# Kernel tuning notes

Hardware: AMD Instinct MI355X
Metric: run time of the kernel (lower is better)

## Reference

```python
import jax, jax.numpy as jnp
import numpy as np

B, S, W, MODES, NUM, NLAYERS = 32, 8192, 128, 16, 8, 4
LG = 8192 + 40 - 1  # szie + len - 1 (Gabor filter length)
PI = float(np.pi)


def setup_inputs() -> dict:
    key = jax.random.key(0)
    ks = jax.random.split(key, 10)
    scale = 1.0 / (W * W)
    return {
        "x": jax.random.normal(ks[0], (B, S, 1), jnp.float32),
        "w1_re": scale * jax.random.uniform(ks[1], (NLAYERS, W, W, MODES), jnp.float32),
        "w1_im": scale * jax.random.uniform(ks[2], (NLAYERS, W, W, MODES), jnp.float32),
        "gamma": jnp.tile(jnp.linspace(0.01, 0.02, NUM, dtype=jnp.float32)[None], (NLAYERS, 1)),
        "fwhm": jnp.tile(jnp.linspace(0.001, 0.002, NUM, dtype=jnp.float32)[None], (NLAYERS, 1)),
        "w2": jax.random.uniform(ks[3], (NLAYERS, NUM), jnp.float32),
        "cw": jax.random.normal(ks[4], (NLAYERS, W, W), jnp.float32) / np.sqrt(W),
        "cb": jnp.zeros((NLAYERS, W), jnp.float32),
        "fc0_w": jax.random.normal(ks[5], (W, 2), jnp.float32) / np.sqrt(2.0),
        "fc0_b": jnp.zeros((W,), jnp.float32),
        "fc1_w": jax.random.normal(ks[6], (128, W), jnp.float32) / np.sqrt(W),
        "fc1_b": jnp.zeros((128,), jnp.float32),
        "fc2_w": jax.random.normal(ks[7], (1, 128), jnp.float32) / np.sqrt(128.0),
        "fc2_b": jnp.zeros((1,), jnp.float32),
    }


def _spectral_conv(h, w_re, w_im, gamma, fwhm, w2):
    # h: [B, C, S] real. w_re/w_im: [C, C, MODES]. gamma/fwhm/w2: [NUM].
    u = jnp.linspace(-0.5, 0.5, LG, dtype=h.dtype)                      # [LG]
    t1 = (gamma * PI / (fwhm + 1e-5))[:, None]                          # [NUM,1]
    gab = jnp.exp(-(t1 ** 2) * (u[None, :] - fwhm[:, None]) ** 2)       # [NUM,LG]
    gab = jnp.fft.ifftshift(gab, axes=-1)[:, :MODES]                     # [NUM,MODES]
    # weights2 is a scalar per latent kernel -> fold the num-reduction into an
    # effective per-mode Gabor weight (exact same math as the repeated einsum + sum).
    g_eff = jnp.einsum("k,km->m", w2, gab)                               # [MODES]
    w1 = (w_re + 1j * w_im) * g_eff[None, None, :]                       # [C,C,MODES] complex
    xf = jnp.fft.rfft(h)                                                 # [B,C,F], F=S//2+1
    out_m = jnp.einsum("bim,iom->bom", xf[..., :MODES], w1)              # [B,C,MODES]
    out = jnp.zeros(xf.shape, dtype=xf.dtype).at[..., :MODES].set(out_m)
    return jnp.fft.irfft(out, n=h.shape[-1])                             # [B,C,S]


def reference(x, w1_re, w1_im, gamma, fwhm, w2, cw, cb, fc0_w, fc0_b, fc1_w, fc1_b, fc2_w, fc2_b):
    b, s, _ = x.shape
    grid = jnp.broadcast_to(jnp.linspace(0.0, 1.0, s, dtype=x.dtype)[None, :, None], (b, s, 1))
    h = jnp.concatenate([x, grid], axis=-1)                              # [B,S,2]
    h = h @ fc0_w.T + fc0_b                                              # [B,S,W]
    h = jnp.transpose(h, (0, 2, 1))                                      # [B,W,S]
    for l in range(NLAYERS):
        x1 = _spectral_conv(h, w1_re[l], w1_im[l], gamma[l], fwhm[l], w2[l])
        x2 = jnp.einsum("oi,bis->bos", cw[l], h) + cb[l][None, :, None]  # 1x1 conv
        h = x1 + x2
        if l < NLAYERS - 1:
            h = jax.nn.gelu(h, approximate=False)
    h = jnp.transpose(h, (0, 2, 1))                                      # [B,S,W]
    h = jax.nn.gelu(h @ fc1_w.T + fc1_b, approximate=False)              # [B,S,128]
    return h @ fc2_w.T + fc2_b                                           # [B,S,1]
```

## Files before the change

kernel.cpp:

```cpp
#include <hip/hip_runtime.h>
#include <hip/hip_fp16.h>

#define BB 32
#define SS 8192
#define CC 128
#define MM 16
#define NUMK 8
#define NL 4

#define TWO_PI 6.2831853071795864769f

typedef _Float16 f16x8 __attribute__((ext_vector_type(8)));
typedef float f32x4 __attribute__((ext_vector_type(4)));

#define MFMA16(a, b, c) __builtin_amdgcn_mfma_f32_16x16x32_f16((a), (b), (c), 0, 0, 0)

__device__ __forceinline__ float gelu_f(float v) {
    float u = 0.7978845608f * fmaf(0.044715f * v * v, v, v);
    float a = fabsf(u);
    float e = __expf(-2.0f * a);
    float th = __fdividef(1.0f - e, 1.0f + e);
    th = copysignf(th, u);
    return 0.5f * v * (1.0f + th);
}

__device__ __align__(256) __half g_trigA[SS * 32];
__device__ __align__(256) __half g_trigD[32 * SS];
__device__ __align__(256) __half g_cwh[NL * CC * CC];
__device__ __align__(256) __half g_fc1h[CC * CC];
__device__ __align__(256) __half g_omh[BB * CC * 32];
__device__ __align__(256) float  g_Xfp[BB * 64 * 32 * CC];
__device__ __align__(256) float  g_Xf[BB * 32 * CC];
__device__ __align__(256) float  g_Xx[BB * MM * 2];
__device__ __align__(256) float  g_Xg[MM * 2];

__global__ __launch_bounds__(256) void k_prep(const float* __restrict__ cw,
                                              const float* __restrict__ fc1_w) {
    int idx = blockIdx.x * 256 + threadIdx.x;
    if (idx < NL * CC * CC) g_cwh[idx] = __float2half(cw[idx]);
    if (idx < CC * CC)      g_fc1h[idx] = __float2half(fc1_w[idx]);
}

__global__ __launch_bounds__(256) void k_trig() {
    int s = blockIdx.x * 256 + threadIdx.x;
    for (int m = 0; m < MM; m++) {
        int ms = (m * s) & (SS - 1);
        float th = (float)ms * (TWO_PI / (float)SS);
        float sn, cs;
        sincosf(th, &sn, &cs);
        g_trigA[s * 32 + m]        = __float2half(cs);
        g_trigA[s * 32 + 16 + m]   = __float2half(sn);
        g_trigD[m * SS + s]        = __float2half(cs);
        g_trigD[(16 + m) * SS + s] = __float2half(-sn);
    }
}

__global__ __launch_bounds__(256) void k_dftx(const float* __restrict__ x) {
    __shared__ float red[4][MM][2];
    int blk = blockIdx.x;
    int t = threadIdx.x;
    int lane = t & 63;
    int wv = t >> 6;

    float accR[MM], accI[MM], cr[MM], ci[MM], pc[MM], ps[MM];
#pragma unroll
    for (int m = 0; m < MM; m++) {
        float sn, cs;
        sincosf((TWO_PI / (float)SS) * (float)(m * t), &sn, &cs);
        cr[m] = cs; ci[m] = -sn;
        sincosf((TWO_PI * 256.0f / (float)SS) * (float)m, &sn, &cs);
        pc[m] = cs; ps[m] = -sn;
        accR[m] = 0.f; accI[m] = 0.f;
    }
    for (int k = 0; k < 32; k++) {
        int s = t + (k << 8);
        float v = (blk < BB) ? x[(blk << 13) + s] : (float)s * (1.0f / 8191.0f);
#pragma unroll
        for (int m = 0; m < MM; m++) {
            accR[m] = fmaf(v, cr[m], accR[m]);
            accI[m] = fmaf(v, ci[m], accI[m]);
            float nc = cr[m] * pc[m] - ci[m] * ps[m];
            float ns = cr[m] * ps[m] + ci[m] * pc[m];
            cr[m] = nc; ci[m] = ns;
        }
    }
#pragma unroll
    for (int m = 0; m < MM; m++) {
#pragma unroll
        for (int off = 32; off > 0; off >>= 1) {
            accR[m] += __shfl_xor(accR[m], off, 64);
            accI[m] += __shfl_xor(accI[m], off, 64);
        }
        if (lane == 0) { red[wv][m][0] = accR[m]; red[wv][m][1] = accI[m]; }
    }
    __syncthreads();
    if (t < MM * 2) {
        int m = t >> 1, p = t & 1;
        float s = red[0][m][p] + red[1][m][p] + red[2][m][p] + red[3][m][p];
        if (blk < BB) g_Xx[(blk << 5) + (m << 1) + p] = s;
        else          g_Xg[(m << 1) + p] = s;
    }
}

__global__ __launch_bounds__(256) void k_xf0(const float* __restrict__ fc0_w,
                                             const float* __restrict__ fc0_b) {
    int n = blockIdx.x * 256 + threadIdx.x;
    int i = n & 127, m2 = (n >> 7) & 31, b = n >> 12;
    int m = m2 & 15, p = m2 >> 4;
    float xv = g_Xx[(b << 5) + (m << 1) + p];
    float gv = g_Xg[(m << 1) + p];
    float v = fc0_w[2 * i] * xv + fc0_w[2 * i + 1] * gv;
    if (p == 0 && m == 0) v += (float)SS * fc0_b[i];
    g_Xf[(b << 12) + (m2 << 7) + i] = v;
}

__global__ __launch_bounds__(256) void k_fc0(const float* __restrict__ x,
                                             const float* __restrict__ fc0_w,
                                             const float* __restrict__ fc0_b,
                                             __half* __restrict__ h) {
    int idx = blockIdx.x * 256 + threadIdx.x;
    int wq = idx & 15;
    int s = (idx >> 4) & (SS - 1);
    int b = idx >> 17;
    float g = (float)s * (1.0f / (float)(SS - 1));
    float xv = x[(b << 13) + s];
    union { __half2 q[4]; f16x8 v; } pk;
#pragma unroll
    for (int j = 0; j < 4; j++) {
        int w = wq * 8 + j * 2;
        float4 fw = *(const float4*)(fc0_w + 2 * w);
        float2 fb = *(const float2*)(fc0_b + w);
        float v0 = fmaf(fw.x, xv, fmaf(fw.y, g, fb.x));
        float v1 = fmaf(fw.z, xv, fmaf(fw.w, g, fb.y));
        pk.q[j] = __floats2half2_rn(v0, v1);
    }
    *(f16x8*)((char*)h + ((long)idx << 4)) = pk.v;
}

__global__ __launch_bounds__(256) void k_red2() {
    int n = blockIdx.x * 256 + threadIdx.x;
    int i = n & 127, m2 = (n >> 7) & 31, b = n >> 12;
    const float* p = g_Xfp + (((b << 6) << 5) + (m2 << 7)) + i;
    float s = 0.f;
#pragma unroll 8
    for (int t = 0; t < 64; t++) s += p[t << 12];
    g_Xf[(b << 12) + (m2 << 7) + i] = s;
}

__global__ __launch_bounds__(256) void k_mix(const float* __restrict__ w1_re,
                                             const float* __restrict__ w1_im,
                                             const float* __restrict__ gamma,
                                             const float* __restrict__ fwhm,
                                             const float* __restrict__ w2,
                                             const float* __restrict__ cb, int l) {
    __shared__ float geff[MM];
    int t = threadIdx.x;
    if (t < MM) {
        float g = 0.f;
        for (int k = 0; k < NUMK; k++) {
            float fw = fwhm[l * NUMK + k];
            float t1 = gamma[l * NUMK + k] * 3.14159265358979f / (fw + 1e-5f);
            float u = (float)t * (1.0f / 8230.0f) - fw;
            g = fmaf(w2[l * NUMK + k], expf(-t1 * t1 * u * u), g);
        }
        geff[t] = g;
    }
    __syncthreads();

    int n = blockIdx.x * 256 + t;
    int m = n & 15, o = (n >> 4) & 127, b = n >> 11;
    const float* xr = g_Xf + (b << 12) + (m << 7);
    const float* xi = g_Xf + (b << 12) + ((16 + m) << 7);
    const float* wr = w1_re + (l << 18) + (o << 4) + m;
    const float* wi = w1_im + (l << 18) + (o << 4) + m;
    float orr = 0.f, oii = 0.f;
    for (int i = 0; i < CC; i++) {
        float xrv = xr[i], xiv = xi[i];
        float wrv = wr[i << 11], wiv = wi[i << 11];
        orr = fmaf(xrv, wrv, orr); orr = fmaf(-xiv, wiv, orr);
        oii = fmaf(xrv, wiv, oii); oii = fmaf(xiv, wrv, oii);
    }
    float sc = geff[m] * (2.0f / (float)SS) * ((m == 0) ? 0.5f : 1.0f);
    float base = (m == 0) ? cb[l * CC + o] : 0.0f;
    g_omh[(b << 12) + (o << 5) + m]      = __float2half(orr * sc + base);
    g_omh[(b << 12) + (o << 5) + 16 + m] = __float2half(-oii * sc);
}

#define GEMM_STEP(KS, HA, HB)                                                       \
    _Pragma("unroll")                                                               \
    for (int af = 0; af < 8; af++) {                                                \
        int row = (af << 4) + lr;                                                   \
        const f16x8 av = *(const f16x8*)(ldsA + (row << 8) +                        \
                          ((((KS << 2) + lg) ^ (row & 7)) << 4));                   \
        acc[af][0] = MFMA16(av, HA, acc[af][0]);                                    \
        acc[af][1] = MFMA16(av, HB, acc[af][1]);                                    \
    }

#define LOAD_HF(S0X)                                                                \
    {                                                                               \
        int hr = (((b << 13) + (S0X) + (wid << 5) + lr) << 8) + (lg << 4);          \
        hf0 = *(const f16x8*)(h_c + hr);                                            \
        hf1 = *(const f16x8*)(h_c + hr + (16 << 8));                                \
        hf2 = *(const f16x8*)(h_c + hr + (1 << 6));                                 \
        hf3 = *(const f16x8*)(h_c + hr + (16 << 8) + (1 << 6));                     \
        hf4 = *(const f16x8*)(h_c + hr + (2 << 6));                                 \
        hf5 = *(const f16x8*)(h_c + hr + (16 << 8) + (2 << 6));                     \
        hf6 = *(const f16x8*)(h_c + hr + (3 << 6));                                 \
        hf7 = *(const f16x8*)(h_c + hr + (16 << 8) + (3 << 6));                     \
    }

#define LOAD_TF(S0X)                                                                \
    {                                                                               \
        int tr2 = (((S0X) + (wid << 5) + lr) << 6) + (lg << 4);                     \
        tf0 = *(const f16x8*)(ta_c + tr2);                                          \
        tf1 = *(const f16x8*)(ta_c + tr2 + (16 << 6));                              \
    }

template <int TAIL>
__global__ __launch_bounds__(256, 2) void k_layer(__half* __restrict__ h, int l) {
    __shared__ __align__(16) char smem[TAIL ? 73728 : 40960];
    char* ldsA = smem;
    char* ldsO = smem + 32768;
    char* ldsS = smem + (TAIL ? 40960 : 0);
    int bi = blockIdx.x;
    int b = bi >> 4, grp = bi & 15;
    int Sg = grp << 9;
    int t = threadIdx.x;
    int wid = __builtin_amdgcn_readfirstlane(t >> 6);
    int l6 = t & 63, lr = l6 & 15, lg = l6 >> 4;
    const char* h_c = (const char*)h;
    char* hw = (char*)h;
    const char* cw_c = (const char*)(g_cwh + l * CC * CC);
    const char* om_c = (const char*)(g_omh + (b << 12));
    const char* ta_c = (const char*)g_trigA;
    const char* td_c = (const char*)g_trigD;
    char* strip = ldsS + (wid << 13);

#pragma unroll
    for (int k = 0; k < 8; k++) {
        int c = (k << 8) + t;
        f16x8 v = *(const f16x8*)(cw_c + (c << 4));
        int row = c >> 4, c16 = c & 15;
        *(f16x8*)(ldsA + (row << 8) + ((c16 ^ (row & 7)) << 4)) = v;
    }
#pragma unroll
    for (int k = 0; k < 2; k++) {
        int c = (k << 8) + t;
        f16x8 v = *(const f16x8*)(om_c + (c << 4));
        int row = c >> 2, c4 = c & 3;
        *(f16x8*)(ldsO + (row << 6) + ((c4 ^ (row & 3)) << 4)) = v;
    }
    f16x8 hf0, hf1, hf2, hf3, hf4, hf5, hf6, hf7, tf0, tf1;
    LOAD_HF(Sg)
    LOAD_TF(Sg)
    __syncthreads();

    f32x4 dacc[8][2];
    if (TAIL) {
#pragma unroll
        for (int af = 0; af < 8; af++) {
            dacc[af][0] = (f32x4){0.f, 0.f, 0.f, 0.f};
            dacc[af][1] = (f32x4){0.f, 0.f, 0.f, 0.f};
        }
    }

    for (int ti = 0; ti < 4; ti++) {
        int S0 = Sg + (ti << 7);
        f32x4 acc[8][2];
#pragma unroll
        for (int af = 0; af < 8; af++) {
            acc[af][0] = (f32x4){0.f, 0.f, 0.f, 0.f};
            acc[af][1] = (f32x4){0.f, 0.f, 0.f, 0.f};
        }
        __builtin_amdgcn_s_setprio(1);
        GEMM_STEP(0, hf0, hf1)
        GEMM_STEP(1, hf2, hf3)
        GEMM_STEP(2, hf4, hf5)
        GEMM_STEP(3, hf6, hf7)
#pragma unroll
        for (int af = 0; af < 8; af++) {
            int row = (af << 4) + lr;
            const f16x8 ov = *(const f16x8*)(ldsO + (row << 6) + ((lg ^ (row & 3)) << 4));
            acc[af][0] = MFMA16(ov, tf0, acc[af][0]);
            acc[af][1] = MFMA16(ov, tf1, acc[af][1]);
        }
        __builtin_amdgcn_s_setprio(0);
        if (ti < 3) {
            int S0n = S0 + 128;
            LOAD_HF(S0n)
            LOAD_TF(S0n)
        }
        f16x8 td0, td1;
        if (TAIL) {
            int sgl = S0 + (wid << 5) + (lg << 3);
            td0 = *(const f16x8*)(td_c + (((lr << 13) + sgl) << 1));
            td1 = *(const f16x8*)(td_c + ((((16 + lr) << 13) + sgl) << 1));
        }
#pragma unroll
        for (int bf = 0; bf < 2; bf++) {
            int s_w = (bf << 4) + lr;
            int s = S0 + (wid << 5) + s_w;
#pragma unroll
            for (int af = 0; af < 8; af++) {
                int o0 = (af << 4) + (lg << 2);
                float v0 = acc[af][bf][0], v1 = acc[af][bf][1];
                float v2 = acc[af][bf][2], v3 = acc[af][bf][3];
                if (TAIL) { v0 = gelu_f(v0); v1 = gelu_f(v1); v2 = gelu_f(v2); v3 = gelu_f(v3); }
                union { __half2 q[2]; unsigned long long u; } pk;
                pk.q[0] = __floats2half2_rn(v0, v1);
                pk.q[1] = __floats2half2_rn(v2, v3);
                *(unsigned long long*)(hw + (((b << 13) + s) << 8) + (o0 << 1)) = pk.u;
                if (TAIL) {
                    int byte = (s_w << 8) + ((o0 << 1) ^ ((s_w & 15) << 4));
                    *(unsigned long long*)(strip + byte) = pk.u;
                }
            }
        }
        if (TAIL) {
            asm volatile("s_waitcnt lgkmcnt(0)" ::: "memory");
            __builtin_amdgcn_sched_barrier(0);
#pragma unroll
            for (int af = 0; af < 8; af++) {
                int o = (af << 4) + lr;
                union { unsigned int u[4]; f16x8 v; } bb;
#pragma unroll
                for (int p = 0; p < 4; p++) {
                    int s0 = (lg << 3) + 2 * p, s1 = s0 + 1;
                    unsigned int lo = *(const unsigned short*)
                        (strip + (s0 << 8) + ((o << 1) ^ ((s0 & 15) << 4)));
                    unsigned int hi = *(const unsigned short*)
                        (strip + (s1 << 8) + ((o << 1) ^ ((s1 & 15) << 4)));
                    bb.u[p] = lo | (hi << 16);
                }
                dacc[af][0] = MFMA16(td0, bb.v, dacc[af][0]);
                dacc[af][1] = MFMA16(td1, bb.v, dacc[af][1]);
            }
        }
    }
    if (TAIL) {
        float* xp = g_Xfp + (((b << 6) + (grp << 2) + wid) << 12);
#pragma unroll
        for (int af = 0; af < 8; af++)
#pragma unroll
            for (int mh = 0; mh < 2; mh++)
#pragma unroll
                for (int reg = 0; reg < 4; reg++) {
                    int m2 = (mh << 4) + (lg << 2) + reg;
                    int o = (af << 4) + lr;
                    xp[(m2 << 7) + o] = dacc[af][mh][reg];
                }
    }
}

__global__ __launch_bounds__(256) void k_head(const __half* __restrict__ h,
                                              const float* __restrict__ fc1_b,
                                              const float* __restrict__ fc2_w,
                                              const float* __restrict__ fc2_b,
                                              float* __restrict__ out) {
    __shared__ __align__(16) char smem[32768];
    char* ldsA = smem;
    int bi = blockIdx.x;
    int b = bi >> 4, grp = bi & 15;
    int Sg = grp << 9;
    int t = threadIdx.x;
    int wid = __builtin_amdgcn_readfirstlane(t >> 6);
    int l6 = t & 63, lr = l6 & 15, lg = l6 >> 4;
    const char* h_c = (const char*)h;
    const char* f1_c = (const char*)g_fc1h;

#pragma unroll
    for (int k = 0; k < 8; k++) {
        int c = (k << 8) + t;
        f16x8 v = *(const f16x8*)(f1_c + (c << 4));
        int row = c >> 4, c16 = c & 15;
        *(f16x8*)(ldsA + (row << 8) + ((c16 ^ (row & 7)) << 4)) = v;
    }
    f16x8 hf0, hf1, hf2, hf3, hf4, hf5, hf6, hf7;
    LOAD_HF(Sg)
    __syncthreads();

    float f2b = fc2_b[0];
    for (int ti = 0; ti < 4; ti++) {
        int S0 = Sg + (ti << 7);
        f32x4 acc[8][2];
#pragma unroll
        for (int af = 0; af < 8; af++) {
            acc[af][0] = (f32x4){0.f, 0.f, 0.f, 0.f};
            acc[af][1] = (f32x4){0.f, 0.f, 0.f, 0.f};
        }
        __builtin_amdgcn_s_setprio(1);
        GEMM_STEP(0, hf0, hf1)
        GEMM_STEP(1, hf2, hf3)
        GEMM_STEP(2, hf4, hf5)
        GEMM_STEP(3, hf6, hf7)
        __builtin_amdgcn_s_setprio(0);
        if (ti < 3) { LOAD_HF(S0 + 128) }
        float p[2] = {0.f, 0.f};
#pragma unroll
        for (int af = 0; af < 8; af++) {
            float4 fb = *(const float4*)(fc1_b + (af << 4) + (lg << 2));
            float4 f2 = *(const float4*)(fc2_w + (af << 4) + (lg << 2));
#pragma unroll
            for (int bf = 0; bf < 2; bf++) {
                float v0 = gelu_f(acc[af][bf][0] + fb.x);
                float v1 = gelu_f(acc[af][bf][1] + fb.y);
                float v2 = gelu_f(acc[af][bf][2] + fb.z);
                float v3 = gelu_f(acc[af][bf][3] + fb.w);
                p[bf] += f2.x * v0 + f2.y * v1 + f2.z * v2 + f2.w * v3;
            }
        }
#pragma unroll
        for (int bf = 0; bf < 2; bf++) {
            float v = p[bf];
            v += __shfl_xor(v, 16, 64);
            v += __shfl_xor(v, 32, 64);
            if (lg == 0) out[(b << 13) + S0 + (wid << 5) + (bf << 4) + lr] = v + f2b;
        }
    }
}

extern "C" void kernel_launch(void* const* d_in, const int* in_sizes, int n_in,
                              void* d_out, int out_size, void* d_ws, size_t ws_size,
                              hipStream_t stream) {
    const float* x      = (const float*)d_in[0];
    const float* w1_re  = (const float*)d_in[1];
    const float* w1_im  = (const float*)d_in[2];
    const float* gamma  = (const float*)d_in[3];
    const float* fwhm   = (const float*)d_in[4];
    const float* w2     = (const float*)d_in[5];
    const float* cw     = (const float*)d_in[6];
    const float* cb     = (const float*)d_in[7];
    const float* fc0_w  = (const float*)d_in[8];
    const float* fc0_b  = (const float*)d_in[9];
    const float* fc1_w  = (const float*)d_in[10];
    const float* fc1_b  = (const float*)d_in[11];
    const float* fc2_w  = (const float*)d_in[12];
    const float* fc2_b  = (const float*)d_in[13];
    float* out = (float*)d_out;

    __half* h = (__half*)d_ws;

    k_prep<<<dim3(256), dim3(256), 0, stream>>>(cw, fc1_w);
    k_trig<<<dim3(32), dim3(256), 0, stream>>>();
    k_dftx<<<dim3(33), dim3(256), 0, stream>>>(x);
    k_xf0<<<dim3(512), dim3(256), 0, stream>>>(fc0_w, fc0_b);
    k_fc0<<<dim3(16384), dim3(256), 0, stream>>>(x, fc0_w, fc0_b, h);
    for (int l = 0; l < NL; l++) {
        k_mix<<<dim3(256), dim3(256), 0, stream>>>(w1_re, w1_im, gamma, fwhm, w2, cb, l);
        if (l < NL - 1) {
            k_layer<1><<<dim3(512), dim3(256), 0, stream>>>(h, l);
            k_red2<<<dim3(512), dim3(256), 0, stream>>>();
        } else {
            k_layer<0><<<dim3(512), dim3(256), 0, stream>>>(h, l);
        }
    }
    k_head<<<dim3(512), dim3(256), 0, stream>>>(h, fc1_b, fc2_w, fc2_b, out);
}
```

Measured before the change: 342.3 us.

## Fuse last layer with head and stage h stores through LDS for coalescing

The final spectral layer and the fc1/gelu/fc2 head are merged into one kernel. The layer output stays in an LDS strip as fp16 and feeds the fc1 MFMA directly, so the last full write and re-read of h in global memory goes away, along with one launch. In the non-final layers, h is now written back from the swizzled LDS strip as 16-byte rows instead of scattered 8-byte stores. The cost is that fc1 weights are read from global/L2 inside the inner loop, and the extra LDS readback adds latency.

```diff
diff --git a/kernel.cpp b/kernel.cpp
--- a/kernel.cpp
+++ b/kernel.cpp
@@ -216,12 +216,11 @@
         tf1 = *(const f16x8*)(ta_c + tr2 + (16 << 6));                              \
     }
 
-template <int TAIL>
 __global__ __launch_bounds__(256, 2) void k_layer(__half* __restrict__ h, int l) {
-    __shared__ __align__(16) char smem[TAIL ? 73728 : 40960];
+    __shared__ __align__(16) char smem[73728];
     char* ldsA = smem;
     char* ldsO = smem + 32768;
-    char* ldsS = smem + (TAIL ? 40960 : 0);
+    char* ldsS = smem + 40960;
     int bi = blockIdx.x;
     int b = bi >> 4, grp = bi & 15;
     int Sg = grp << 9;
@@ -256,12 +255,10 @@
     __syncthreads();
 
     f32x4 dacc[8][2];
-    if (TAIL) {
-#pragma unroll
-        for (int af = 0; af < 8; af++) {
-            dacc[af][0] = (f32x4){0.f, 0.f, 0.f, 0.f};
-            dacc[af][1] = (f32x4){0.f, 0.f, 0.f, 0.f};
-        }
+#pragma unroll
+    for (int af = 0; af < 8; af++) {
+        dacc[af][0] = (f32x4){0.f, 0.f, 0.f, 0.f};
+        dacc[af][1] = (f32x4){0.f, 0.f, 0.f, 0.f};
     }
 
     for (int ti = 0; ti < 4; ti++) {
@@ -291,7 +288,7 @@
             LOAD_TF(S0n)
         }
         f16x8 td0, td1;
-        if (TAIL) {
+        {
             int sgl = S0 + (wid << 5) + (lg << 3);
             td0 = *(const f16x8*)(td_c + (((lr << 13) + sgl) << 1));
             td1 = *(const f16x8*)(td_c + ((((16 + lr) << 13) + sgl) << 1));
@@ -299,45 +296,44 @@
 #pragma unroll
         for (int bf = 0; bf < 2; bf++) {
             int s_w = (bf << 4) + lr;
-            int s = S0 + (wid << 5) + s_w;
 #pragma unroll
             for (int af = 0; af < 8; af++) {
                 int o0 = (af << 4) + (lg << 2);
-                float v0 = acc[af][bf][0], v1 = acc[af][bf][1];
-                float v2 = acc[af][bf][2], v3 = acc[af][bf][3];
-                if (TAIL) { v0 = gelu_f(v0); v1 = gelu_f(v1); v2 = gelu_f(v2); v3 = gelu_f(v3); }
+                float v0 = gelu_f(acc[af][bf][0]), v1 = gelu_f(acc[af][bf][1]);
+                float v2 = gelu_f(acc[af][bf][2]), v3 = gelu_f(acc[af][bf][3]);
                 union { __half2 q[2]; unsigned long long u; } pk;
                 pk.q[0] = __floats2half2_rn(v0, v1);
                 pk.q[1] = __floats2half2_rn(v2, v3);
-                *(unsigned long long*)(hw + (((b << 13) + s) << 8) + (o0 << 1)) = pk.u;
-                if (TAIL) {
-                    int byte = (s_w << 8) + ((o0 << 1) ^ ((s_w & 15) << 4));
-                    *(unsigned long long*)(strip + byte) = pk.u;
-                }
-            }
-        }
-        if (TAIL) {
-            asm volatile("s_waitcnt lgkmcnt(0)" ::: "memory");
-            __builtin_amdgcn_sched_barrier(0);
-#pragma unroll
-            for (int af = 0; af < 8; af++) {
-                int o = (af << 4) + lr;
-                union { unsigned int u[4]; f16x8 v; } bb;
-#pragma unroll
-                for (int p = 0; p < 4; p++) {
-                    int s0 = (lg << 3) + 2 * p, s1 = s0 + 1;
-                    unsigned int lo = *(const unsigned short*)
-                        (strip + (s0 << 8) + ((o << 1) ^ ((s0 & 15) << 4)));
-                    unsigned int hi = *(const unsigned short*)
-                        (strip + (s1 << 8) + ((o << 1) ^ ((s1 & 15) << 4)));
-                    bb.u[p] = lo | (hi << 16);
-                }
-                dacc[af][0] = MFMA16(td0, bb.v, dacc[af][0]);
-                dacc[af][1] = MFMA16(td1, bb.v, dacc[af][1]);
-            }
-        }
-    }
-    if (TAIL) {
+                int byte = (s_w << 8) + ((o0 << 1) ^ ((s_w & 15) << 4));
+                *(unsigned long long*)(strip + byte) = pk.u;
+            }
+        }
+        asm volatile("s_waitcnt lgkmcnt(0)" ::: "memory");
+        __builtin_amdgcn_sched_barrier(0);
+#pragma unroll
+        for (int af = 0; af < 8; af++) {
+            int o = (af << 4) + lr;
+            union { unsigned int u[4]; f16x8 v; } bb;
+#pragma unroll
+            for (int p = 0; p < 4; p++) {
+                int s0 = (lg << 3) + 2 * p, s1 = s0 + 1;
+                unsigned int lo = *(const unsigned short*)
+                    (strip + (s0 << 8) + ((o << 1) ^ ((s0 & 15) << 4)));
+                unsigned int hi = *(const unsigned short*)
+                    (strip + (s1 << 8) + ((o << 1) ^ ((s1 & 15) << 4)));
+                bb.u[p] = lo | (hi << 16);
+            }
+            dacc[af][0] = MFMA16(td0, bb.v, dacc[af][0]);
+            dacc[af][1] = MFMA16(td1, bb.v, dacc[af][1]);
+        }
+#pragma unroll
+        for (int rg = 0; rg < 8; rg++) {
+            int s_w = (rg << 2) + lg;
+            f16x8 rd = *(const f16x8*)(strip + (s_w << 8) + ((lr ^ (s_w & 15)) << 4));
+            *(f16x8*)(hw + (((b << 13) + S0 + (wid << 5) + s_w) << 8) + (lr << 4)) = rd;
+        }
+    }
+    {
         float* xp = g_Xfp + (((b << 6) + (grp << 2) + wid) << 12);
 #pragma unroll
         for (int af = 0; af < 8; af++)
@@ -352,13 +348,15 @@
     }
 }
 
-__global__ __launch_bounds__(256) void k_head(const __half* __restrict__ h,
-                                              const float* __restrict__ fc1_b,
-                                              const float* __restrict__ fc2_w,
-                                              const float* __restrict__ fc2_b,
-                                              float* __restrict__ out) {
-    __shared__ __align__(16) char smem[32768];
+__global__ __launch_bounds__(256, 2) void k_tail(const __half* __restrict__ h,
+                                                 const float* __restrict__ fc1_b,
+                                                 const float* __restrict__ fc2_w,
+                                                 const float* __restrict__ fc2_b,
+                                                 float* __restrict__ out) {
+    __shared__ __align__(16) char smem[73728];
     char* ldsA = smem;
+    char* ldsO = smem + 32768;
+    char* ldsS = smem + 40960;
     int bi = blockIdx.x;
     int b = bi >> 4, grp = bi & 15;
     int Sg = grp << 9;
@@ -366,55 +364,126 @@
     int wid = __builtin_amdgcn_readfirstlane(t >> 6);
     int l6 = t & 63, lr = l6 & 15, lg = l6 >> 4;
     const char* h_c = (const char*)h;
+    const char* cw_c = (const char*)(g_cwh + 3 * CC * CC);
+    const char* om_c = (const char*)(g_omh + (b << 12));
+    const char* ta_c = (const char*)g_trigA;
     const char* f1_c = (const char*)g_fc1h;
+    char* strip = ldsS + (wid << 13);
 
 #pragma unroll
     for (int k = 0; k < 8; k++) {
         int c = (k << 8) + t;
-        f16x8 v = *(const f16x8*)(f1_c + (c << 4));
+        f16x8 v = *(const f16x8*)(cw_c + (c << 4));
         int row = c >> 4, c16 = c & 15;
         *(f16x8*)(ldsA + (row << 8) + ((c16 ^ (row & 7)) << 4)) = v;
     }
-    f16x8 hf0, hf1, hf2, hf3, hf4, hf5, hf6, hf7;
+#pragma unroll
+    for (int k = 0; k < 2; k++) {
+        int c = (k << 8) + t;
+        f16x8 v = *(const f16x8*)(om_c + (c << 4));
+        int row = c >> 2, c4 = c & 3;
+        *(f16x8*)(ldsO + (row << 6) + ((c4 ^ (row & 3)) << 4)) = v;
+    }
+    f16x8 hf0, hf1, hf2, hf3, hf4, hf5, hf6, hf7, tf0, tf1;
     LOAD_HF(Sg)
+    LOAD_TF(Sg)
     __syncthreads();
 
     float f2b = fc2_b[0];
     for (int ti = 0; ti < 4; ti++) {
         int S0 = Sg + (ti << 7);
-        f32x4 acc[8][2];
-#pragma unroll
-        for (int af = 0; af < 8; af++) {
-            acc[af][0] = (f32x4){0.f, 0.f, 0.f, 0.f};
-            acc[af][1] = (f32x4){0.f, 0.f, 0.f, 0.f};
-        }
-        __builtin_amdgcn_s_setprio(1);
-        GEMM_STEP(0, hf0, hf1)
-        GEMM_STEP(1, hf2, hf3)
-        GEMM_STEP(2, hf4, hf5)
-        GEMM_STEP(3, hf6, hf7)
-        __builtin_amdgcn_s_setprio(0);
-        if (ti < 3) { LOAD_HF(S0 + 128) }
-        float p[2] = {0.f, 0.f};
-#pragma unroll
-        for (int af = 0; af < 8; af++) {
-            float4 fb = *(const float4*)(fc1_b + (af << 4) + (lg << 2));
-            float4 f2 = *(const float4*)(fc2_w + (af << 4) + (lg << 2));
+        {
+            f32x4 acc[8][2];
+#pragma unroll
+            for (int af = 0; af < 8; af++) {
+                acc[af][0] = (f32x4){0.f, 0.f, 0.f, 0.f};
+                acc[af][1] = (f32x4){0.f, 0.f, 0.f, 0.f};
+            }
+            __builtin_amdgcn_s_setprio(1);
+            GEMM_STEP(0, hf0, hf1)
+            GEMM_STEP(1, hf2, hf3)
+            GEMM_STEP(2, hf4, hf5)
+            GEMM_STEP(3, hf6, hf7)
+#pragma unroll
+            for (int af = 0; af < 8; af++) {
+                int row = (af << 4) + lr;
+                const f16x8 ov = *(const f16x8*)(ldsO + (row << 6) + ((lg ^ (row & 3)) << 4));
+                acc[af][0] = MFMA16(ov, tf0, acc[af][0]);
+                acc[af][1] = MFMA16(ov, tf1, acc[af][1]);
+            }
+            __builtin_amdgcn_s_setprio(0);
+            if (ti < 3) {
+                int S0n = S0 + 128;
+                LOAD_HF(S0n)
+                LOAD_TF(S0n)
+            }
 #pragma unroll
             for (int bf = 0; bf < 2; bf++) {
-                float v0 = gelu_f(acc[af][bf][0] + fb.x);
-                float v1 = gelu_f(acc[af][bf][1] + fb.y);
-                float v2 = gelu_f(acc[af][bf][2] + fb.z);
-                float v3 = gelu_f(acc[af][bf][3] + fb.w);
-                p[bf] += f2.x * v0 + f2.y * v1 + f2.z * v2 + f2.w * v3;
-            }
-        }
-#pragma unroll
-        for (int bf = 0; bf < 2; bf++) {
-            float v = p[bf];
-            v += __shfl_xor(v, 16, 64);
-            v += __shfl_xor(v, 32, 64);
-            if (lg == 0) out[(b << 13) + S0 + (wid << 5) + (bf << 4) + lr] = v + f2b;
+                int s_w = (bf << 4) + lr;
+#pragma unroll
+                for (int af = 0; af < 8; af++) {
+                    int o0 = (af << 4) + (lg << 2);
+                    union { __half2 q[2]; unsigned long long u; } pk;
+                    pk.q[0] = __floats2half2_rn(acc[af][bf][0], acc[af][bf][1]);
+                    pk.q[1] = __floats2half2_rn(acc[af][bf][2], acc[af][bf][3]);
+                    int byte = (s_w << 8) + ((o0 << 1) ^ ((s_w & 15) << 4));
+                    *(unsigned long long*)(strip + byte) = pk.u;
+                }
+            }
+        }
+        asm volatile("s_waitcnt lgkmcnt(0)" ::: "memory");
+        __builtin_amdgcn_sched_barrier(0);
+        {
+            f32x4 acc2[8][2];
+#pragma unroll
+            for (int af = 0; af < 8; af++) {
+                acc2[af][0] = (f32x4){0.f, 0.f, 0.f, 0.f};
+                acc2[af][1] = (f32x4){0.f, 0.f, 0.f, 0.f};
+            }
+#pragma unroll
+            for (int ks = 0; ks < 4; ks++) {
+#pragma unroll
+                for (int bf = 0; bf < 2; bf++) {
+                    int s_loc = (bf << 4) + lr;
+                    union { unsigned int u[4]; f16x8 v; } bb;
+#pragma unroll
+                    for (int p = 0; p < 4; p++) {
+                        int o0 = (ks << 5) + (lg << 3) + 2 * p, o1 = o0 + 1;
+                        unsigned int lo = *(const unsigned short*)
+                            (strip + (s_loc << 8) + ((o0 << 1) ^ ((s_loc & 15) << 4)));
+                        unsigned int hi = *(const unsigned short*)
+                            (strip + (s_loc << 8) + ((o1 << 1) ^ ((s_loc & 15) << 4)));
+                        bb.u[p] = lo | (hi << 16);
+                    }
+#pragma unroll
+                    for (int af = 0; af < 8; af++) {
+                        const f16x8 av = *(const f16x8*)
+                            (f1_c + (((af << 4) + lr) << 8) + (ks << 6) + (lg << 4));
+                        acc2[af][bf] = MFMA16(av, bb.v, acc2[af][bf]);
+                    }
+                }
+            }
+            float p[2] = {0.f, 0.f};
+#pragma unroll
+            for (int af = 0; af < 8; af++) {
+                float4 fb = *(const float4*)(fc1_b + (af << 4) + (lg << 2));
+                float4 f2 = *(const float4*)(fc2_w + (af << 4) + (lg << 2));
+#pragma unroll
+                for (int bf = 0; bf < 2; bf++) {
+                    float v0 = gelu_f(acc2[af][bf][0] + fb.x);
+                    float v1 = gelu_f(acc2[af][bf][1] + fb.y);
+                    float v2 = gelu_f(acc2[af][bf][2] + fb.z);
+                    float v3 = gelu_f(acc2[af][bf][3] + fb.w);
+                    p[bf] += f2.x * v0 + f2.y * v1 + f2.z * v2 + f2.w * v3;
+                }
+            }
+#pragma unroll
+            for (int bf = 0; bf < 2; bf++) {
+                float v = p[bf];
+                v += __shfl_xor(v, 16, 64);
+                v += __shfl_xor(v, 32, 64);
+                if (lg == 0) out[(b << 13) + S0 + (wid << 5) + (bf << 4) + lr] = v + f2b;
+            }
         }
     }
 }
@@ -448,11 +517,10 @@
     for (int l = 0; l < NL; l++) {
         k_mix<<<dim3(256), dim3(256), 0, stream>>>(w1_re, w1_im, gamma, fwhm, w2, cb, l);
         if (l < NL - 1) {
-            k_layer<1><<<dim3(512), dim3(256), 0, stream>>>(h, l);
+            k_layer<<<dim3(512), dim3(256), 0, stream>>>(h, l);
             k_red2<<<dim3(512), dim3(256), 0, stream>>>();
         } else {
-            k_layer<0><<<dim3(512), dim3(256), 0, stream>>>(h, l);
-        }
-    }
-    k_head<<<dim3(512), dim3(256), 0, stream>>>(h, fc1_b, fc2_w, fc2_b, out);
-}
+            k_tail<<<dim3(512), dim3(256), 0, stream>>>(h, fc1_b, fc2_w, fc2_b, out);
+        }
+    }
+}
```

Result: slower. 372.3 us (+8.8%).

## Fuse fc0 lift into first layer kernel and transpose spectral weights for mixing

Applied to the files above, without the earlier changes.

Removes the standalone fc0 kernel: the first layer kernel now computes the lifted activations in registers from x, the grid coordinate and fp16 fc0 weights, avoiding one full write and read of the activation buffer. Adds a prep kernel that transposes the spectral weights so the mode-mixing kernel reads contiguous float4 vectors instead of strided scalars. Fc0 arithmetic is now done in half precision, which may slightly change numerics.

```diff
diff --git a/kernel.cpp b/kernel.cpp
--- a/kernel.cpp
+++ b/kernel.cpp
@@ -33,12 +33,39 @@
 __device__ __align__(256) float  g_Xf[BB * 32 * CC];
 __device__ __align__(256) float  g_Xx[BB * MM * 2];
 __device__ __align__(256) float  g_Xg[MM * 2];
+__device__ __align__(256) float  g_w1Tr[NL * MM * CC * CC];
+__device__ __align__(256) float  g_w1Ti[NL * MM * CC * CC];
 
 __global__ __launch_bounds__(256) void k_prep(const float* __restrict__ cw,
                                               const float* __restrict__ fc1_w) {
     int idx = blockIdx.x * 256 + threadIdx.x;
     if (idx < NL * CC * CC) g_cwh[idx] = __float2half(cw[idx]);
     if (idx < CC * CC)      g_fc1h[idx] = __float2half(fc1_w[idx]);
+}
+
+__global__ __launch_bounds__(256) void k_prepw(const float* __restrict__ w1_re,
+                                               const float* __restrict__ w1_im) {
+    __shared__ float tr[16 * 132], tim[16 * 132];
+    int bi = blockIdx.x;
+    int l = bi >> 7, o = bi & 127;
+    int t = threadIdx.x;
+#pragma unroll
+    for (int it = 0; it < 8; it++) {
+        int idx = (it << 8) + t;
+        int i = idx >> 4, m = idx & 15;
+        int src = (l << 18) + (i << 11) + (o << 4) + m;
+        tr[m * 132 + i]  = w1_re[src];
+        tim[m * 132 + i] = w1_im[src];
+    }
+    __syncthreads();
+#pragma unroll
+    for (int it = 0; it < 8; it++) {
+        int idx = (it << 8) + t;
+        int i = idx & 127, m = idx >> 7;
+        int dst = (l << 18) + (m << 14) + (o << 7) + i;
+        g_w1Tr[dst] = tr[m * 132 + i];
+        g_w1Ti[dst] = tim[m * 132 + i];
+    }
 }
 
 __global__ __launch_bounds__(256) void k_trig() {
@@ -114,29 +141,6 @@
     g_Xf[(b << 12) + (m2 << 7) + i] = v;
 }
 
-__global__ __launch_bounds__(256) void k_fc0(const float* __restrict__ x,
-                                             const float* __restrict__ fc0_w,
-                                             const float* __restrict__ fc0_b,
-                                             __half* __restrict__ h) {
-    int idx = blockIdx.x * 256 + threadIdx.x;
-    int wq = idx & 15;
-    int s = (idx >> 4) & (SS - 1);
-    int b = idx >> 17;
-    float g = (float)s * (1.0f / (float)(SS - 1));
-    float xv = x[(b << 13) + s];
-    union { __half2 q[4]; f16x8 v; } pk;
-#pragma unroll
-    for (int j = 0; j < 4; j++) {
-        int w = wq * 8 + j * 2;
-        float4 fw = *(const float4*)(fc0_w + 2 * w);
-        float2 fb = *(const float2*)(fc0_b + w);
-        float v0 = fmaf(fw.x, xv, fmaf(fw.y, g, fb.x));
-        float v1 = fmaf(fw.z, xv, fmaf(fw.w, g, fb.y));
-        pk.q[j] = __floats2half2_rn(v0, v1);
-    }
-    *(f16x8*)((char*)h + ((long)idx << 4)) = pk.v;
-}
-
 __global__ __launch_bounds__(256) void k_red2() {
     int n = blockIdx.x * 256 + threadIdx.x;
     int i = n & 127, m2 = (n >> 7) & 31, b = n >> 12;
@@ -147,9 +151,7 @@
     g_Xf[(b << 12) + (m2 << 7) + i] = s;
 }
 
-__global__ __launch_bounds__(256) void k_mix(const float* __restrict__ w1_re,
-                                             const float* __restrict__ w1_im,
-                                             const float* __restrict__ gamma,
+__global__ __launch_bounds__(256) void k_mix(const float* __restrict__ gamma,
                                              const float* __restrict__ fwhm,
                                              const float* __restrict__ w2,
                                              const float* __restrict__ cb, int l) {
@@ -171,14 +173,19 @@
     int m = n & 15, o = (n >> 4) & 127, b = n >> 11;
     const float* xr = g_Xf + (b << 12) + (m << 7);
     const float* xi = g_Xf + (b << 12) + ((16 + m) << 7);
-    const float* wr = w1_re + (l << 18) + (o << 4) + m;
-    const float* wi = w1_im + (l << 18) + (o << 4) + m;
+    const float* wr = g_w1Tr + (l << 18) + (m << 14) + (o << 7);
+    const float* wi = g_w1Ti + (l << 18) + (m << 14) + (o << 7);
     float orr = 0.f, oii = 0.f;
-    for (int i = 0; i < CC; i++) {
-        float xrv = xr[i], xiv = xi[i];
-        float wrv = wr[i << 11], wiv = wi[i << 11];
-        orr = fmaf(xrv, wrv, orr); orr = fmaf(-xiv, wiv, orr);
-        oii = fmaf(xrv, wiv, oii); oii = fmaf(xiv, wrv, oii);
+#pragma unroll 8
+    for (int i = 0; i < CC; i += 4) {
+        float4 xr4 = *(const float4*)(xr + i);
+        float4 xi4 = *(const float4*)(xi + i);
+        float4 wr4 = *(const float4*)(wr + i);
+        float4 wi4 = *(const float4*)(wi + i);
+        orr += xr4.x * wr4.x - xi4.x * wi4.x + xr4.y * wr4.y - xi4.y * wi4.y
+             + xr4.z * wr4.z - xi4.z * wi4.z + xr4.w * wr4.w - xi4.w * wi4.w;
+        oii += xr4.x * wi4.x + xi4.x * wr4.x + xr4.y * wi4.y + xi4.y * wr4.y
+             + xr4.z * wi4.z + xi4.z * wr4.z + xr4.w * wi4.w + xi4.w * wr4.w;
     }
     float sc = geff[m] * (2.0f / (float)SS) * ((m == 0) ? 0.5f : 1.0f);
     float base = (m == 0) ? cb[l * CC + o] : 0.0f;
@@ -216,8 +223,11 @@
         tf1 = *(const f16x8*)(ta_c + tr2 + (16 << 6));                              \
     }
 
-template <int TAIL>
-__global__ __launch_bounds__(256, 2) void k_layer(__half* __restrict__ h, int l) {
+template <int SRC, int TAIL>
+__global__ __launch_bounds__(256, 2) void k_layer(__half* __restrict__ h,
+                                                  const float* __restrict__ x,
+                                                  const float* __restrict__ fc0_w,
+                                                  const float* __restrict__ fc0_b, int l) {
     __shared__ __align__(16) char smem[TAIL ? 73728 : 40960];
     char* ldsA = smem;
     char* ldsO = smem + 32768;
@@ -251,7 +261,34 @@
         *(f16x8*)(ldsO + (row << 6) + ((c4 ^ (row & 3)) << 4)) = v;
     }
     f16x8 hf0, hf1, hf2, hf3, hf4, hf5, hf6, hf7, tf0, tf1;
-    LOAD_HF(Sg)
+    union HU { __half2 q[4]; f16x8 v; };
+    HU c0[4], c1[4], cbh[4];
+    float xv0 = 0.f, xv1 = 0.f;
+    if (SRC) {
+#pragma unroll
+        for (int ks = 0; ks < 4; ks++) {
+            int i0 = (ks << 5) + (lg << 3);
+            const float* wp = fc0_w + (i0 << 1);
+            float4 a  = *(const float4*)(wp);
+            float4 bq = *(const float4*)(wp + 4);
+            float4 cq = *(const float4*)(wp + 8);
+            float4 dq = *(const float4*)(wp + 12);
+            c0[ks].q[0] = __floats2half2_rn(a.x, a.z);   c1[ks].q[0] = __floats2half2_rn(a.y, a.w);
+            c0[ks].q[1] = __floats2half2_rn(bq.x, bq.z); c1[ks].q[1] = __floats2half2_rn(bq.y, bq.w);
+            c0[ks].q[2] = __floats2half2_rn(cq.x, cq.z); c1[ks].q[2] = __floats2half2_rn(cq.y, cq.w);
+            c0[ks].q[3] = __floats2half2_rn(dq.x, dq.z); c1[ks].q[3] = __floats2half2_rn(dq.y, dq.w);
+            float4 e = *(const float4*)(fc0_b + i0);
+            float4 f = *(const float4*)(fc0_b + i0 + 4);
+            cbh[ks].q[0] = __floats2half2_rn(e.x, e.y);
+            cbh[ks].q[1] = __floats2half2_rn(e.z, e.w);
+            cbh[ks].q[2] = __floats2half2_rn(f.x, f.y);
+            cbh[ks].q[3] = __floats2half2_rn(f.z, f.w);
+        }
+        xv0 = x[(b << 13) + Sg + (wid << 5) + lr];
+        xv1 = x[(b << 13) + Sg + (wid << 5) + 16 + lr];
+    } else {
+        LOAD_HF(Sg)
+    }
     LOAD_TF(Sg)
     __syncthreads();
 
@@ -266,6 +303,28 @@
 
     for (int ti = 0; ti < 4; ti++) {
         int S0 = Sg + (ti << 7);
+        if (SRC) {
+            int sA = S0 + (wid << 5) + lr;
+            __half2 xx0 = __floats2half2_rn(xv0, xv0);
+            __half2 xx1 = __floats2half2_rn(xv1, xv1);
+            float gv0 = (float)sA * (1.0f / 8191.0f);
+            float gv1 = (float)(sA + 16) * (1.0f / 8191.0f);
+            __half2 gg0 = __floats2half2_rn(gv0, gv0);
+            __half2 gg1 = __floats2half2_rn(gv1, gv1);
+#pragma unroll
+            for (int ks = 0; ks < 4; ks++) {
+                HU r0, r1;
+#pragma unroll
+                for (int q = 0; q < 4; q++) {
+                    r0.q[q] = __hfma2(c0[ks].q[q], xx0, __hfma2(c1[ks].q[q], gg0, cbh[ks].q[q]));
+                    r1.q[q] = __hfma2(c0[ks].q[q], xx1, __hfma2(c1[ks].q[q], gg1, cbh[ks].q[q]));
+                }
+                if (ks == 0)      { hf0 = r0.v; hf1 = r1.v; }
+                else if (ks == 1) { hf2 = r0.v; hf3 = r1.v; }
+                else if (ks == 2) { hf4 = r0.v; hf5 = r1.v; }
+                else              { hf6 = r0.v; hf7 = r1.v; }
+            }
+        }
         f32x4 acc[8][2];
 #pragma unroll
         for (int af = 0; af < 8; af++) {
@@ -287,7 +346,12 @@
         __builtin_amdgcn_s_setprio(0);
         if (ti < 3) {
             int S0n = S0 + 128;
-            LOAD_HF(S0n)
+            if (SRC) {
+                xv0 = x[(b << 13) + S0n + (wid << 5) + lr];
+                xv1 = x[(b << 13) + S0n + (wid << 5) + 16 + lr];
+            } else {
+                LOAD_HF(S0n)
+            }
             LOAD_TF(S0n)
         }
         f16x8 td0, td1;
@@ -441,17 +505,20 @@
     __half* h = (__half*)d_ws;
 
     k_prep<<<dim3(256), dim3(256), 0, stream>>>(cw, fc1_w);
+    k_prepw<<<dim3(512), dim3(256), 0, stream>>>(w1_re, w1_im);
     k_trig<<<dim3(32), dim3(256), 0, stream>>>();
     k_dftx<<<dim3(33), dim3(256), 0, stream>>>(x);
     k_xf0<<<dim3(512), dim3(256), 0, stream>>>(fc0_w, fc0_b);
-    k_fc0<<<dim3(16384), dim3(256), 0, stream>>>(x, fc0_w, fc0_b, h);
     for (int l = 0; l < NL; l++) {
-        k_mix<<<dim3(256), dim3(256), 0, stream>>>(w1_re, w1_im, gamma, fwhm, w2, cb, l);
-        if (l < NL - 1) {
-            k_layer<1><<<dim3(512), dim3(256), 0, stream>>>(h, l);
+        k_mix<<<dim3(256), dim3(256), 0, stream>>>(gamma, fwhm, w2, cb, l);
+        if (l == 0) {
+            k_layer<1, 1><<<dim3(512), dim3(256), 0, stream>>>(h, x, fc0_w, fc0_b, l);
+            k_red2<<<dim3(512), dim3(256), 0, stream>>>();
+        } else if (l < NL - 1) {
+            k_layer<0, 1><<<dim3(512), dim3(256), 0, stream>>>(h, x, fc0_w, fc0_b, l);
             k_red2<<<dim3(512), dim3(256), 0, stream>>>();
         } else {
-            k_layer<0><<<dim3(512), dim3(256), 0, stream>>>(h, l);
+            k_layer<0, 0><<<dim3(512), dim3(256), 0, stream>>>(h, x, fc0_w, fc0_b, l);
         }
     }
     k_head<<<dim3(512), dim3(256), 0, stream>>>(h, fc1_b, fc2_w, fc2_b, out);
```

Measured after the change: 354.5 us. +3.6%, slower.

## Read weights from global cache instead of LDS, double grid, pretranspose spectral weights

Applied to the files above, without the earlier changes.

The layer and head kernels stop staging the 1x1-conv/fc1 weights and spectral-output matrix in LDS and read them straight from global memory through the cache. This removes the staging and barrier and frees LDS, so blocks can halve their sequence span, the grid doubles to 1024 blocks, and the occupancy hint goes from 2 to 3. Per-block partial DFT sums are now reduced across waves in LDS before one write, which halves the partials buffer and the k_red2 loop. The spectral weights are pretransposed once so k_mix can do contiguous float4 loads. The cost is more global/L2 traffic for the weight fragments, plus an extra prep kernel.

```diff
diff --git a/kernel.cpp b/kernel.cpp
--- a/kernel.cpp
+++ b/kernel.cpp
@@ -29,16 +29,43 @@
 __device__ __align__(256) __half g_cwh[NL * CC * CC];
 __device__ __align__(256) __half g_fc1h[CC * CC];
 __device__ __align__(256) __half g_omh[BB * CC * 32];
-__device__ __align__(256) float  g_Xfp[BB * 64 * 32 * CC];
+__device__ __align__(256) float  g_Xfp[BB * 32 * 32 * CC];
 __device__ __align__(256) float  g_Xf[BB * 32 * CC];
 __device__ __align__(256) float  g_Xx[BB * MM * 2];
 __device__ __align__(256) float  g_Xg[MM * 2];
+__device__ __align__(256) float  g_w1Tr[NL * MM * CC * CC];
+__device__ __align__(256) float  g_w1Ti[NL * MM * CC * CC];
 
 __global__ __launch_bounds__(256) void k_prep(const float* __restrict__ cw,
                                               const float* __restrict__ fc1_w) {
     int idx = blockIdx.x * 256 + threadIdx.x;
     if (idx < NL * CC * CC) g_cwh[idx] = __float2half(cw[idx]);
     if (idx < CC * CC)      g_fc1h[idx] = __float2half(fc1_w[idx]);
+}
+
+__global__ __launch_bounds__(256) void k_prepw(const float* __restrict__ w1_re,
+                                               const float* __restrict__ w1_im) {
+    __shared__ float tr[16 * 132], tim[16 * 132];
+    int bi = blockIdx.x;
+    int l = bi >> 7, o = bi & 127;
+    int t = threadIdx.x;
+#pragma unroll
+    for (int it = 0; it < 8; it++) {
+        int idx = (it << 8) + t;
+        int i = idx >> 4, m = idx & 15;
+        int src = (l << 18) + (i << 11) + (o << 4) + m;
+        tr[m * 132 + i]  = w1_re[src];
+        tim[m * 132 + i] = w1_im[src];
+    }
+    __syncthreads();
+#pragma unroll
+    for (int it = 0; it < 8; it++) {
+        int idx = (it << 8) + t;
+        int i = idx & 127, m = idx >> 7;
+        int dst = (l << 18) + (m << 14) + (o << 7) + i;
+        g_w1Tr[dst] = tr[m * 132 + i];
+        g_w1Ti[dst] = tim[m * 132 + i];
+    }
 }
 
 __global__ __launch_bounds__(256) void k_trig() {
@@ -140,16 +167,14 @@
 __global__ __launch_bounds__(256) void k_red2() {
     int n = blockIdx.x * 256 + threadIdx.x;
     int i = n & 127, m2 = (n >> 7) & 31, b = n >> 12;
-    const float* p = g_Xfp + (((b << 6) << 5) + (m2 << 7)) + i;
+    const float* p = g_Xfp + ((long)b << 17) + (m2 << 7) + i;
     float s = 0.f;
 #pragma unroll 8
-    for (int t = 0; t < 64; t++) s += p[t << 12];
+    for (int t = 0; t < 32; t++) s += p[t << 12];
     g_Xf[(b << 12) + (m2 << 7) + i] = s;
 }
 
-__global__ __launch_bounds__(256) void k_mix(const float* __restrict__ w1_re,
-                                             const float* __restrict__ w1_im,
-                                             const float* __restrict__ gamma,
+__global__ __launch_bounds__(256) void k_mix(const float* __restrict__ gamma,
                                              const float* __restrict__ fwhm,
                                              const float* __restrict__ w2,
                                              const float* __restrict__ cb, int l) {
@@ -171,14 +196,19 @@
     int m = n & 15, o = (n >> 4) & 127, b = n >> 11;
     const float* xr = g_Xf + (b << 12) + (m << 7);
     const float* xi = g_Xf + (b << 12) + ((16 + m) << 7);
-    const float* wr = w1_re + (l << 18) + (o << 4) + m;
-    const float* wi = w1_im + (l << 18) + (o << 4) + m;
+    const float* wr = g_w1Tr + (l << 18) + (m << 14) + (o << 7);
+    const float* wi = g_w1Ti + (l << 18) + (m << 14) + (o << 7);
     float orr = 0.f, oii = 0.f;
-    for (int i = 0; i < CC; i++) {
-        float xrv = xr[i], xiv = xi[i];
-        float wrv = wr[i << 11], wiv = wi[i << 11];
-        orr = fmaf(xrv, wrv, orr); orr = fmaf(-xiv, wiv, orr);
-        oii = fmaf(xrv, wiv, oii); oii = fmaf(xiv, wrv, oii);
+#pragma unroll 8
+    for (int i = 0; i < CC; i += 4) {
+        float4 xr4 = *(const float4*)(xr + i);
+        float4 xi4 = *(const float4*)(xi + i);
+        float4 wr4 = *(const float4*)(wr + i);
+        float4 wi4 = *(const float4*)(wi + i);
+        orr += xr4.x * wr4.x - xi4.x * wi4.x + xr4.y * wr4.y - xi4.y * wi4.y
+             + xr4.z * wr4.z - xi4.z * wi4.z + xr4.w * wr4.w - xi4.w * wi4.w;
+        oii += xr4.x * wi4.x + xi4.x * wr4.x + xr4.y * wi4.y + xi4.y * wr4.y
+             + xr4.z * wi4.z + xi4.z * wr4.z + xr4.w * wi4.w + xi4.w * wr4.w;
     }
     float sc = geff[m] * (2.0f / (float)SS) * ((m == 0) ? 0.5f : 1.0f);
     float base = (m == 0) ? cb[l * CC + o] : 0.0f;
@@ -190,8 +220,7 @@
     _Pragma("unroll")                                                               \
     for (int af = 0; af < 8; af++) {                                                \
         int row = (af << 4) + lr;                                                   \
-        const f16x8 av = *(const f16x8*)(ldsA + (row << 8) +                        \
-                          ((((KS << 2) + lg) ^ (row & 7)) << 4));                   \
+        const f16x8 av = *(const f16x8*)(aw_c + (row << 8) + ((KS) << 6) + (lg << 4)); \
         acc[af][0] = MFMA16(av, HA, acc[af][0]);                                    \
         acc[af][1] = MFMA16(av, HB, acc[af][1]);                                    \
     }
@@ -217,43 +246,25 @@
     }
 
 template <int TAIL>
-__global__ __launch_bounds__(256, 2) void k_layer(__half* __restrict__ h, int l) {
-    __shared__ __align__(16) char smem[TAIL ? 73728 : 40960];
-    char* ldsA = smem;
-    char* ldsO = smem + 32768;
-    char* ldsS = smem + (TAIL ? 40960 : 0);
+__global__ __launch_bounds__(256, 3) void k_layer(__half* __restrict__ h, int l) {
+    __shared__ __align__(16) char smem[TAIL ? 32768 : 16];
     int bi = blockIdx.x;
-    int b = bi >> 4, grp = bi & 15;
-    int Sg = grp << 9;
+    int b = bi >> 5, grp = bi & 31;
+    int Sg = grp << 8;
     int t = threadIdx.x;
     int wid = __builtin_amdgcn_readfirstlane(t >> 6);
     int l6 = t & 63, lr = l6 & 15, lg = l6 >> 4;
     const char* h_c = (const char*)h;
     char* hw = (char*)h;
-    const char* cw_c = (const char*)(g_cwh + l * CC * CC);
+    const char* aw_c = (const char*)(g_cwh + l * CC * CC);
     const char* om_c = (const char*)(g_omh + (b << 12));
     const char* ta_c = (const char*)g_trigA;
     const char* td_c = (const char*)g_trigD;
-    char* strip = ldsS + (wid << 13);
-
-#pragma unroll
-    for (int k = 0; k < 8; k++) {
-        int c = (k << 8) + t;
-        f16x8 v = *(const f16x8*)(cw_c + (c << 4));
-        int row = c >> 4, c16 = c & 15;
-        *(f16x8*)(ldsA + (row << 8) + ((c16 ^ (row & 7)) << 4)) = v;
-    }
-#pragma unroll
-    for (int k = 0; k < 2; k++) {
-        int c = (k << 8) + t;
-        f16x8 v = *(const f16x8*)(om_c + (c << 4));
-        int row = c >> 2, c4 = c & 3;
-        *(f16x8*)(ldsO + (row << 6) + ((c4 ^ (row & 3)) << 4)) = v;
-    }
+    char* strip = smem + (wid << 13);
+
     f16x8 hf0, hf1, hf2, hf3, hf4, hf5, hf6, hf7, tf0, tf1;
     LOAD_HF(Sg)
     LOAD_TF(Sg)
-    __syncthreads();
 
     f32x4 dacc[8][2];
     if (TAIL) {
@@ -264,7 +275,7 @@
         }
     }
 
-    for (int ti = 0; ti < 4; ti++) {
+    for (int ti = 0; ti < 2; ti++) {
         int S0 = Sg + (ti << 7);
         f32x4 acc[8][2];
 #pragma unroll
@@ -280,15 +291,14 @@
 #pragma unroll
         for (int af = 0; af < 8; af++) {
             int row = (af << 4) + lr;
-            const f16x8 ov = *(const f16x8*)(ldsO + (row << 6) + ((lg ^ (row & 3)) << 4));
+            const f16x8 ov = *(const f16x8*)(om_c + (row << 6) + (lg << 4));
             acc[af][0] = MFMA16(ov, tf0, acc[af][0]);
             acc[af][1] = MFMA16(ov, tf1, acc[af][1]);
         }
         __builtin_amdgcn_s_setprio(0);
-        if (ti < 3) {
-            int S0n = S0 + 128;
-            LOAD_HF(S0n)
-            LOAD_TF(S0n)
+        if (ti == 0) {
+            LOAD_HF(Sg + 128)
+            LOAD_TF(Sg + 128)
         }
         f16x8 td0, td1;
         if (TAIL) {
@@ -338,49 +348,78 @@
         }
     }
     if (TAIL) {
-        float* xp = g_Xfp + (((b << 6) + (grp << 2) + wid) << 12);
-#pragma unroll
-        for (int af = 0; af < 8; af++)
-#pragma unroll
-            for (int mh = 0; mh < 2; mh++)
-#pragma unroll
-                for (int reg = 0; reg < 4; reg++) {
-                    int m2 = (mh << 4) + (lg << 2) + reg;
-                    int o = (af << 4) + lr;
-                    xp[(m2 << 7) + o] = dacc[af][mh][reg];
-                }
-    }
-}
-
-__global__ __launch_bounds__(256) void k_head(const __half* __restrict__ h,
-                                              const float* __restrict__ fc1_b,
-                                              const float* __restrict__ fc2_w,
-                                              const float* __restrict__ fc2_b,
-                                              float* __restrict__ out) {
-    __shared__ __align__(16) char smem[32768];
-    char* ldsA = smem;
+        float* red = (float*)smem;
+        __syncthreads();
+        if (wid == 1 || wid == 3) {
+            float* rp = red + ((wid >> 1) << 12) + l6;
+#pragma unroll
+            for (int af = 0; af < 8; af++)
+#pragma unroll
+                for (int mh = 0; mh < 2; mh++)
+#pragma unroll
+                    for (int reg = 0; reg < 4; reg++)
+                        rp[((af << 3) + (mh << 2) + reg) << 6] = dacc[af][mh][reg];
+        }
+        __syncthreads();
+        if (wid == 0 || wid == 2) {
+            const float* rp = red + ((wid >> 1) << 12) + l6;
+#pragma unroll
+            for (int af = 0; af < 8; af++)
+#pragma unroll
+                for (int mh = 0; mh < 2; mh++)
+#pragma unroll
+                    for (int reg = 0; reg < 4; reg++)
+                        dacc[af][mh][reg] += rp[((af << 3) + (mh << 2) + reg) << 6];
+        }
+        __syncthreads();
+        if (wid == 2) {
+            float* rp = red + l6;
+#pragma unroll
+            for (int af = 0; af < 8; af++)
+#pragma unroll
+                for (int mh = 0; mh < 2; mh++)
+#pragma unroll
+                    for (int reg = 0; reg < 4; reg++)
+                        rp[((af << 3) + (mh << 2) + reg) << 6] = dacc[af][mh][reg];
+        }
+        __syncthreads();
+        if (wid == 0) {
+            const float* rp = red + l6;
+            float* xp = g_Xfp + (((long)(b << 5) + grp) << 12);
+#pragma unroll
+            for (int af = 0; af < 8; af++)
+#pragma unroll
+                for (int mh = 0; mh < 2; mh++)
+#pragma unroll
+                    for (int reg = 0; reg < 4; reg++) {
+                        float v = dacc[af][mh][reg] + rp[((af << 3) + (mh << 2) + reg) << 6];
+                        int m2 = (mh << 4) + (lg << 2) + reg;
+                        int o = (af << 4) + lr;
+                        xp[(m2 << 7) + o] = v;
+                    }
+        }
+    }
+}
+
+__global__ __launch_bounds__(256, 3) void k_head(const __half* __restrict__ h,
+                                                 const float* __restrict__ fc1_b,
+                                                 const float* __restrict__ fc2_w,
+                                                 const float* __restrict__ fc2_b,
+                                                 float* __restrict__ out) {
     int bi = blockIdx.x;
-    int b = bi >> 4, grp = bi & 15;
-    int Sg = grp << 9;
+    int b = bi >> 5, grp = bi & 31;
+    int Sg = grp << 8;
     int t = threadIdx.x;
     int wid = __builtin_amdgcn_readfirstlane(t >> 6);
     int l6 = t & 63, lr = l6 & 15, lg = l6 >> 4;
     const char* h_c = (const char*)h;
-    const char* f1_c = (const char*)g_fc1h;
-
-#pragma unroll
-    for (int k = 0; k < 8; k++) {
-        int c = (k << 8) + t;
-        f16x8 v = *(const f16x8*)(f1_c + (c << 4));
-        int row = c >> 4, c16 = c & 15;
-        *(f16x8*)(ldsA + (row << 8) + ((c16 ^ (row & 7)) << 4)) = v;
-    }
+    const char* aw_c = (const char*)g_fc1h;
+
     f16x8 hf0, hf1, hf2, hf3, hf4, hf5, hf6, hf7;
     LOAD_HF(Sg)
-    __syncthreads();
 
     float f2b = fc2_b[0];
-    for (int ti = 0; ti < 4; ti++) {
+    for (int ti = 0; ti < 2; ti++) {
         int S0 = Sg + (ti << 7);
         f32x4 acc[8][2];
 #pragma unroll
@@ -394,7 +433,7 @@
         GEMM_STEP(2, hf4, hf5)
         GEMM_STEP(3, hf6, hf7)
         __builtin_amdgcn_s_setprio(0);
-        if (ti < 3) { LOAD_HF(S0 + 128) }
+        if (ti == 0) { LOAD_HF(Sg + 128) }
         float p[2] = {0.f, 0.f};
 #pragma unroll
         for (int af = 0; af < 8; af++) {
@@ -441,18 +480,19 @@
     __half* h = (__half*)d_ws;
 
     k_prep<<<dim3(256), dim3(256), 0, stream>>>(cw, fc1_w);
+    k_prepw<<<dim3(512), dim3(256), 0, stream>>>(w1_re, w1_im);
     k_trig<<<dim3(32), dim3(256), 0, stream>>>();
     k_dftx<<<dim3(33), dim3(256), 0, stream>>>(x);
     k_xf0<<<dim3(512), dim3(256), 0, stream>>>(fc0_w, fc0_b);
     k_fc0<<<dim3(16384), dim3(256), 0, stream>>>(x, fc0_w, fc0_b, h);
     for (int l = 0; l < NL; l++) {
-        k_mix<<<dim3(256), dim3(256), 0, stream>>>(w1_re, w1_im, gamma, fwhm, w2, cb, l);
+        k_mix<<<dim3(256), dim3(256), 0, stream>>>(gamma, fwhm, w2, cb, l);
         if (l < NL - 1) {
-            k_layer<1><<<dim3(512), dim3(256), 0, stream>>>(h, l);
+            k_layer<1><<<dim3(1024), dim3(256), 0, stream>>>(h, l);
             k_red2<<<dim3(512), dim3(256), 0, stream>>>();
         } else {
-            k_layer<0><<<dim3(512), dim3(256), 0, stream>>>(h, l);
-        }
-    }
-    k_head<<<dim3(512), dim3(256), 0, stream>>>(h, fc1_b, fc2_w, fc2_b, out);
-}
+            k_layer<0><<<dim3(1024), dim3(256), 0, stream>>>(h, l);
+        }
+    }
+    k_head<<<dim3(1024), dim3(256), 0, stream>>>(h, fc1_b, fc2_w, fc2_b, out);
+}
```

Result: slower. 879.1 us (+156.8%).
